# Kernel optimization log

Hardware: AMD Instinct MI355X
Metric: run time of the kernel (lower is better)

## Reference

```python
import jax, jax.numpy as jnp
import numpy as np

B, T, L = 64, 60, 49
EMBED, HID, VOCAB = 768, 768, 10000


def setup_inputs() -> dict:
    key = jax.random.key(0)
    ks = jax.random.split(key, 17)
    def n(k, shape, s=1.0):
        return jax.random.normal(k, shape, dtype=jnp.float32) * s
    W = 0.02  # param init scale
    return {
        "x": n(ks[0], (B, T, 2 * EMBED)),
        "hiddens": n(ks[1], (B, T, HID)),
        "cells": n(ks[2], (B, T, HID)),
        "G": n(ks[3], (B, L, HID)),
        "H": n(ks[4], (B, L, HID)),
        # Sentinel params (bias=False)
        "W_sx": n(ks[5], (HID, 2 * EMBED), W),
        "W_sh": n(ks[6], (HID, HID), W),
        # SwitchableAttention params
        "W_ax": n(ks[7], (HID, 2 * EMBED), W),
        "W_ah": n(ks[8], (HID, HID), W),
        "W_ag": n(ks[9], (HID, HID), W),
        "w_switch": n(ks[10], (1, HID), W),
        # Atten (adaptive attention) params, bias=False
        "Wv": n(ks[11], (L, HID), W),
        "Wg": n(ks[12], (L, HID), W),
        "Ws": n(ks[13], (L, HID), W),
        "wh": n(ks[14], (1, L), W),
        # output MLP
        "W_mlp": n(ks[15], (VOCAB, HID), W),
        "b_mlp": jnp.zeros((VOCAB,), dtype=jnp.float32),
    }


def reference(x, hiddens, cells, G, H, W_sx, W_sh, W_ax, W_ah, W_ag,
              w_switch, Wv, Wg, Ws, wh, W_mlp, b_mlp):
    # Dropout layers are treated as identity (eval mode).
    b, t, _ = x.shape
    # h_{t-1}: zero initial hidden prepended, last step dropped
    h0 = jnp.zeros((b, 1, HID), dtype=hiddens.dtype)
    hiddens_t_1 = jnp.concatenate([h0, hiddens[:, :-1, :]], axis=1)

    # Sentinel gate: sigmoid(Wx x + Wh h_{t-1}) * tanh(c_t)
    gate = jax.nn.sigmoid(jnp.einsum('bte,he->bth', x, W_sx)
                          + jnp.einsum('btk,hk->bth', hiddens_t_1, W_sh))
    s_t = gate * jnp.tanh(cells)  # [B,T,HID]

    # SwitchableAttention: gate between visual H and guidance G per region,
    # conditioned on pooled word context x.
    q = jnp.einsum('bte,he->bth', x, W_ax).mean(axis=1)  # [B,HID]
    sH = jnp.einsum('blh,oh->blo', jnp.tanh(jnp.einsum('blh,kh->blk', H, W_ah) + q[:, None, :]), w_switch)  # [B,L,1]
    sG = jnp.einsum('blh,oh->blo', jnp.tanh(jnp.einsum('blh,kh->blk', G, W_ag) + q[:, None, :]), w_switch)  # [B,L,1]
    switch_weights = jax.nn.softmax(jnp.concatenate([sH, sG], axis=-1), axis=-1)  # [B,L,2]
    V = switch_weights[..., 0:1] * H + switch_weights[..., 1:2] * G  # [B,L,HID]

    # Adaptive attention (Atten): spatial attention + visual sentinel
    pv = jnp.einsum('blh,kh->blk', V, Wv)        # [B,L,49]
    pg = jnp.einsum('bth,kh->btk', hiddens, Wg)  # [B,T,49]
    z_t = jnp.einsum('btlk,ok->btlo', jnp.tanh(pv[:, None, :, :] + pg[:, :, None, :]), wh)[..., 0]  # [B,T,L]
    alpha = jax.nn.softmax(z_t, axis=-1)  # [B,T,L]
    z_s = jnp.einsum('btk,ok->bto', jnp.tanh(jnp.einsum('bth,kh->btk', s_t, Ws) + pg), wh)  # [B,T,1]
    alpha_hat = jax.nn.softmax(jnp.concatenate([z_t, z_s], axis=-1), axis=-1)  # [B,T,L+1]
    beta = alpha_hat[..., -1:]  # [B,T,1]
    c_t = jnp.einsum('btl,blh->bth', alpha, V)
    c_hat = beta * s_t + (1.0 - beta) * c_t

    scores = jnp.einsum('bth,vh->btv', c_hat + hiddens, W_mlp) + b_mlp  # [B,T,VOCAB]
    return scores, alpha, beta, switch_weights
```

## Files before the change

### kernel.cpp

```cpp
#include <hip/hip_runtime.h>

#define BB 64
#define TT 60
#define LL 49
#define HID 768
#define E2 1536
#define K2 2304
#define VOC 10000
#define BT (BB*TT)
#define BL (BB*LL)
#define NPAD_MLP 10240
#define NPAD_S 128

typedef __bf16 bf16x8 __attribute__((ext_vector_type(8)));
typedef float f32x4 __attribute__((ext_vector_type(4)));

__device__ __forceinline__ unsigned short f2bf(float f) {
  union { float f; unsigned int u; } v; v.f = f;
  unsigned int u = v.u;
  return (unsigned short)((u + 0x7fffu + ((u >> 16) & 1u)) >> 16);
}
__device__ __forceinline__ float bf2f(unsigned short h) {
  union { unsigned int u; float f; } v; v.u = ((unsigned int)h) << 16;
  return v.f;
}
__device__ __forceinline__ float fast_tanh(float x) {
  float e = __expf(2.f * x);
  return 1.f - 2.f / (e + 1.f);
}
__device__ __forceinline__ float fast_sigmoid(float x) {
  return 1.f / (1.f + __expf(-x));
}

#define NSEG 14
#define CHUNK4 2048
struct SegT {
  const float* src;
  unsigned short* dst;
  int n4, rl4, dstride4, dcol4, nrows, mode, blk0;
};
struct SegTable { SegT s[NSEG]; };

__global__ __launch_bounds__(256) void k_convall(SegTable tab) {
  int b = blockIdx.x;
  int si = 0;
#pragma unroll
  for (int i = 1; i < NSEG; ++i) si += (b >= tab.s[i].blk0);
  SegT sg = tab.s[si];
  int lb = b - sg.blk0;
  int end = (lb + 1) * CHUNK4; end = end < sg.n4 ? end : sg.n4;
  for (int i = lb * CHUNK4 + threadIdx.x; i < end; i += 256) {
    int row = i / sg.rl4, c = i - row * sg.rl4;
    ushort4 o; o.x = o.y = o.z = o.w = 0;
    if (sg.mode == 0) {
      float4 v = ((const float4*)sg.src)[i];
      o.x = f2bf(v.x); o.y = f2bf(v.y); o.z = f2bf(v.z); o.w = f2bf(v.w);
    } else if (sg.mode == 1) {
      if (row < sg.nrows) {
        float4 v = ((const float4*)sg.src)[i];
        o.x = f2bf(v.x); o.y = f2bf(v.y); o.z = f2bf(v.z); o.w = f2bf(v.w);
      }
    } else {
      if (row % TT != 0) {
        float4 v = ((const float4*)sg.src)[i - sg.rl4];
        o.x = f2bf(v.x); o.y = f2bf(v.y); o.z = f2bf(v.z); o.w = f2bf(v.w);
      }
    }
    ((ushort4*)sg.dst)[(size_t)row * sg.dstride4 + sg.dcol4 + c] = o;
  }
}

__global__ __launch_bounds__(256) void k_xmean(const float* __restrict__ x,
                                               unsigned short* __restrict__ xm) {
  int b = blockIdx.x / 6;
  int c = (blockIdx.x % 6) * 256 + threadIdx.x;
  float s = 0.f;
  for (int t = 0; t < TT; ++t) s += x[((size_t)b * TT + t) * E2 + c];
  xm[(size_t)b * E2 + c] = f2bf(s * (1.f / 60.f));
}

struct SSeg {
  const unsigned short* A; const unsigned short* B;
  float* C; const float* bias; const float* aux; unsigned short* outbf;
  int M, Nout, K, nMblk, blk0, emode;
};
#define NSSEG 4
struct SSegTable { SSeg s[NSSEG]; };

__global__ __launch_bounds__(256) void gemm_bt64_seg(SSegTable tab)
{
  __shared__ __attribute__((aligned(16))) unsigned short As[128*32];
  __shared__ __attribute__((aligned(16))) unsigned short Bs[64*32];
  const int tid  = threadIdx.x;
  const int lane = tid & 63;
  const int wave = tid >> 6;

  const int nwg = gridDim.x;
  const int id  = blockIdx.x;
  const int q = nwg >> 3, r = nwg & 7;
  const int xcd = id & 7, lo = id >> 3;
  const int wgid = (xcd < r ? xcd * (q + 1) : r * (q + 1) + (xcd - r) * q) + lo;

  int si = 0;
#pragma unroll
  for (int i = 1; i < NSSEG; ++i) si += (wgid >= tab.s[i].blk0);
  const SSeg sg = tab.s[si];
  const int lwg = wgid - sg.blk0;
  const int mb = lwg % sg.nMblk;
  const int nb = lwg / sg.nMblk;
  const int M = sg.M, Nout = sg.Nout, K = sg.K;
  const unsigned short* __restrict__ A  = sg.A;
  const unsigned short* __restrict__ Bw = sg.B;
  const int m0 = mb * 128;
  const int n0 = nb * 64;
  const int wm = (wave & 1) * 64;
  const int wn = (wave >> 1) * 32;

  f32x4 acc[4][2];
#pragma unroll
  for (int i = 0; i < 4; ++i)
#pragma unroll
    for (int j = 0; j < 2; ++j) acc[i][j] = f32x4{0.f, 0.f, 0.f, 0.f};

  const int lrow = lane & 15;
  const int kb   = (lane >> 4) * 8;

  for (int k0 = 0; k0 < K; k0 += 32) {
    __syncthreads();
#pragma unroll
    for (int p = 0; p < 2; ++p) {
      int slot = p * 256 + wave * 64 + lane;
      int row = slot >> 2, c8 = slot & 3;
      int ar = m0 + row; ar = ar < M ? ar : (M - 1);
      const unsigned short* asrc = A + (size_t)ar * K + k0 + c8 * 8;
      __builtin_amdgcn_global_load_lds(
          (const __attribute__((address_space(1))) void*)asrc,
          (__attribute__((address_space(3))) void*)&As[slot * 8],
          16, 0, 0);
    }
    {
      int slot = wave * 64 + lane;
      int row = slot >> 2, c8 = slot & 3;
      const unsigned short* bsrc = Bw + (size_t)(n0 + row) * K + k0 + c8 * 8;
      __builtin_amdgcn_global_load_lds(
          (const __attribute__((address_space(1))) void*)bsrc,
          (__attribute__((address_space(3))) void*)&Bs[slot * 8],
          16, 0, 0);
    }
    __syncthreads();

    bf16x8 av[4], bv[2];
#pragma unroll
    for (int i = 0; i < 4; ++i)
      av[i] = *(const bf16x8*)&As[(wm + i * 16 + lrow) * 32 + kb];
#pragma unroll
    for (int j = 0; j < 2; ++j)
      bv[j] = *(const bf16x8*)&Bs[(wn + j * 16 + lrow) * 32 + kb];
#pragma unroll
    for (int i = 0; i < 4; ++i)
#pragma unroll
      for (int j = 0; j < 2; ++j)
        acc[i][j] = __builtin_amdgcn_mfma_f32_16x16x32_bf16(av[i], bv[j], acc[i][j], 0, 0, 0);
  }

  const int cr = (lane >> 4) * 4;
  const int cc = lane & 15;
  if (sg.emode == 0) {
    float* __restrict__ C = sg.C;
    const float* __restrict__ bias = sg.bias;
#pragma unroll
    for (int i = 0; i < 4; ++i) {
      int row0 = m0 + wm + i * 16 + cr;
#pragma unroll
      for (int j = 0; j < 2; ++j) {
        int col = n0 + wn + j * 16 + cc;
        if (col < Nout) {
          float badd = bias ? bias[col] : 0.f;
#pragma unroll
          for (int r2 = 0; r2 < 4; ++r2) {
            int row = row0 + r2;
            if (row < M) C[(size_t)row * Nout + col] = acc[i][j][r2] + badd;
          }
        }
      }
    }
  } else if (sg.emode == 1) {
    const float* __restrict__ cells = sg.aux;
    unsigned short* __restrict__ ob = sg.outbf;
#pragma unroll
    for (int i = 0; i < 4; ++i) {
      int row0 = m0 + wm + i * 16 + cr;
#pragma unroll
      for (int j = 0; j < 2; ++j) {
        int col = n0 + wn + j * 16 + cc;
        if (col < Nout) {
#pragma unroll
          for (int r2 = 0; r2 < 4; ++r2) {
            int row = row0 + r2;
            if (row < M) {
              float cv = cells[(size_t)row * Nout + col];
              ob[(size_t)row * Nout + col] = f2bf(fast_sigmoid(acc[i][j][r2]) * fast_tanh(cv));
            }
          }
        }
      }
    }
  } else {
    unsigned short* __restrict__ ob = sg.outbf;
#pragma unroll
    for (int i = 0; i < 4; ++i) {
      int row0 = m0 + wm + i * 16 + cr;
#pragma unroll
      for (int j = 0; j < 2; ++j) {
        int col = n0 + wn + j * 16 + cc;
        if (col < Nout) {
#pragma unroll
          for (int r2 = 0; r2 < 4; ++r2) {
            int row = row0 + r2;
            if (row < M) ob[(size_t)row * Nout + col] = f2bf(acc[i][j][r2]);
          }
        }
      }
    }
  }
}

#define VM6() asm volatile("s_waitcnt vmcnt(6)" ::: "memory")
#define VM0() asm volatile("s_waitcnt vmcnt(0)" ::: "memory")
#define BARR() do { asm volatile("" ::: "memory"); __builtin_amdgcn_s_barrier(); \
                    asm volatile("" ::: "memory"); } while (0)

#define SC_STAGE(bufi, kt) do {                                                 \
  int k0_ = (kt) * 32;                                                          \
  _Pragma("unroll")                                                             \
  for (int l_ = 0; l_ < 2; ++l_) {                                              \
    int rr_ = l_ * 64 + wave * 16 + (lane >> 2);                                \
    int ss_ = (lane & 3) ^ ((rr_ >> 1) & 3);                                    \
    const unsigned short* src_ = Ap + (size_t)(m0 + rr_) * K + k0_ + ss_ * 8;   \
    char* dst_ = smem + (bufi) * 24576 + l_ * 4096 + wave * 1024;               \
    __builtin_amdgcn_global_load_lds(                                           \
        (const __attribute__((address_space(1))) void*)src_,                    \
        (__attribute__((address_space(3))) void*)dst_, 16, 0, 0);               \
  }                                                                             \
  _Pragma("unroll")                                                             \
  for (int l_ = 0; l_ < 4; ++l_) {                                              \
    int rr_ = l_ * 64 + wave * 16 + (lane >> 2);                                \
    int ss_ = (lane & 3) ^ ((rr_ >> 1) & 3);                                    \
    const unsigned short* src_ = Bw + (size_t)(n0 + rr_) * K + k0_ + ss_ * 8;   \
    char* dst_ = smem + (bufi) * 24576 + 8192 + l_ * 4096 + wave * 1024;        \
    __builtin_amdgcn_global_load_lds(                                           \
        (const __attribute__((address_space(1))) void*)src_,                    \
        (__attribute__((address_space(3))) void*)dst_, 16, 0, 0);               \
  }                                                                             \
} while (0)

#define SC_LDA(bufi, row) (*(const bf16x8*)(smem + (bufi) * 24576 + (row) * 64 + ((cg ^ (((row) >> 1) & 3)) * 16)))
#define SC_LDB(bufi, row) (*(const bf16x8*)(smem + (bufi) * 24576 + 8192 + (row) * 64 + ((cg ^ (((row) >> 1) & 3)) * 16)))

#define SC_TILE(bufi, STAGE_STMT, VM_STMT) do {                                 \
  STAGE_STMT;                                                                   \
  bf16x8 afr0 = SC_LDA(bufi, wm + lrow);                                        \
  bf16x8 afr1 = SC_LDA(bufi, wm + 16 + lrow);                                   \
  bf16x8 afr2 = SC_LDA(bufi, wm + 32 + lrow);                                   \
  bf16x8 afr3 = SC_LDA(bufi, wm + 48 + lrow);                                   \
  __builtin_amdgcn_s_setprio(1);                                                \
  _Pragma("unroll")                                                             \
  for (int j_ = 0; j_ < 8; ++j_) {                                              \
    bf16x8 b_ = SC_LDB(bufi, wn + j_ * 16 + lrow);                              \
    acc[0][j_] = __builtin_amdgcn_mfma_f32_16x16x32_bf16(afr0, b_, acc[0][j_], 0, 0, 0); \
    acc[1][j_] = __builtin_amdgcn_mfma_f32_16x16x32_bf16(afr1, b_, acc[1][j_], 0, 0, 0); \
    acc[2][j_] = __builtin_amdgcn_mfma_f32_16x16x32_bf16(afr2, b_, acc[2][j_], 0, 0, 0); \
    acc[3][j_] = __builtin_amdgcn_mfma_f32_16x16x32_bf16(afr3, b_, acc[3][j_], 0, 0, 0); \
  }                                                                             \
  __builtin_amdgcn_s_setprio(0);                                                \
  VM_STMT;                                                                      \
  BARR();                                                                       \
} while (0)

__global__ __launch_bounds__(256, 2) void gemm_sc2(
    const unsigned short* __restrict__ Ap,
    const unsigned short* __restrict__ Bw,
    float* __restrict__ C,
    const float* __restrict__ bias,
    int M, int Nout, int K, int nMblk)
{
  extern __shared__ char smem[];
  const int tid  = threadIdx.x;
  const int lane = tid & 63;
  const int wave = tid >> 6;
  const int lrow = lane & 15;
  const int cg   = lane >> 4;

  const int nwg = gridDim.x;
  const int id  = blockIdx.x;
  const int q = nwg >> 3, r = nwg & 7;
  const int xcd = id & 7, lo = id >> 3;
  const int wgid = (xcd < r ? xcd * (q + 1) : r * (q + 1) + (xcd - r) * q) + lo;
  const int mb = wgid % nMblk;
  const int nb = wgid / nMblk;

  const int m0 = mb * 128;
  const int n0 = nb * 256;
  const int wm = (wave >> 1) * 64;
  const int wn = (wave & 1) * 128;

  f32x4 acc[4][8];
#pragma unroll
  for (int i = 0; i < 4; ++i)
#pragma unroll
    for (int j = 0; j < 8; ++j) acc[i][j] = f32x4{0.f, 0.f, 0.f, 0.f};

  const int NT = K >> 5;

  SC_STAGE(0, 0);
  SC_STAGE(1, 1);
  VM6();
  BARR();

  int b = 0;
  for (int kt = 0; kt < NT - 2; ++kt) {
    int b2 = b + 2; if (b2 >= 3) b2 -= 3;
    SC_TILE(b, SC_STAGE(b2, kt + 2), VM6(););
    ++b; if (b == 3) b = 0;
  }
  SC_TILE(b, ;, VM0(););
  ++b; if (b == 3) b = 0;
  SC_TILE(b, ;, ;);

#pragma unroll
  for (int i = 0; i < 4; ++i) {
    int row0 = m0 + wm + i * 16 + (lane >> 4) * 4;
#pragma unroll
    for (int j = 0; j < 8; ++j) {
      int col = n0 + wn + j * 16 + (lane & 15);
      if (col < Nout) {
        float badd = bias ? bias[col] : 0.f;
#pragma unroll
        for (int r2 = 0; r2 < 4; ++r2)
          C[(size_t)(row0 + r2) * Nout + col] = acc[i][j][r2] + badd;
      }
    }
  }
}

__global__ __launch_bounds__(256) void k_switch(
    const unsigned short* __restrict__ AH, const unsigned short* __restrict__ AG,
    const float* __restrict__ q, const float* __restrict__ wsw,
    const float* __restrict__ H, const float* __restrict__ G,
    unsigned short* __restrict__ Vbf, float* __restrict__ sw_out)
{
  int bl = blockIdx.x;
  int b = bl / LL;
  int tid = threadIdx.x;
  float aH = 0.f, aG = 0.f;
  for (int h = tid; h < HID; h += 256) {
    float qv = q[b * HID + h], w = wsw[h];
    aH += fast_tanh(bf2f(AH[(size_t)bl * HID + h]) + qv) * w;
    aG += fast_tanh(bf2f(AG[(size_t)bl * HID + h]) + qv) * w;
  }
#pragma unroll
  for (int off = 32; off > 0; off >>= 1) {
    aH += __shfl_down(aH, off);
    aG += __shfl_down(aG, off);
  }
  __shared__ float redH[4], redG[4];
  int lane = tid & 63, wave = tid >> 6;
  if (lane == 0) { redH[wave] = aH; redG[wave] = aG; }
  __syncthreads();
  float sH = redH[0] + redH[1] + redH[2] + redH[3];
  float sG = redG[0] + redG[1] + redG[2] + redG[3];
  float m = fmaxf(sH, sG);
  float e0 = __expf(sH - m), e1 = __expf(sG - m);
  float inv = 1.f / (e0 + e1);
  float sw0 = e0 * inv, sw1 = e1 * inv;
  if (tid == 0) { sw_out[bl * 2] = sw0; sw_out[bl * 2 + 1] = sw1; }
  for (int h = tid; h < HID; h += 256) {
    float v = sw0 * H[(size_t)bl * HID + h] + sw1 * G[(size_t)bl * HID + h];
    Vbf[(size_t)bl * HID + h] = f2bf(v);
  }
}

__global__ __launch_bounds__(256) void k_attn(
    const float* __restrict__ PV, const float* __restrict__ PG,
    const float* __restrict__ SS, const float* __restrict__ wh,
    const unsigned short* __restrict__ stbf, const unsigned short* __restrict__ Vbf,
    const float* __restrict__ hiddens,
    float* __restrict__ alpha_out, float* __restrict__ beta_out,
    unsigned short* __restrict__ chh)
{
  const int TG = 4;
  int b  = blockIdx.x / (TT / TG);
  int t0 = (blockIdx.x % (TT / TG)) * TG;
  int tid = threadIdx.x;
  __shared__ float pg_s[TG][LL], wh_s[LL], zz[TG][LL + 1], alpha_s[TG][LL], beta_sh[TG];

  if (tid < LL) wh_s[tid] = wh[tid];
  if (tid < TG * LL) {
    int tt = tid / LL, k = tid - tt * LL;
    pg_s[tt][k] = PG[(size_t)(b * TT + t0 + tt) * 64 + k];
  }
  __syncthreads();

  if (tid < TG * (LL + 1)) {
    int tt = tid / (LL + 1), l = tid - tt * (LL + 1);
    const float* src = (l < LL) ? &PV[((size_t)b * LL + l) * 64]
                                : &SS[(size_t)(b * TT + t0 + tt) * 64];
    float acc = 0.f;
    for (int k = 0; k < LL; ++k) acc += fast_tanh(src[k] + pg_s[tt][k]) * wh_s[k];
    zz[tt][l] = acc;
  }
  __syncthreads();

  if (tid < TG) {
    int tt = tid, bt = b * TT + t0 + tt;
    float mx = -1e30f;
    for (int l = 0; l < LL; ++l) mx = fmaxf(mx, zz[tt][l]);
    float sum = 0.f;
    for (int l = 0; l < LL; ++l) { float e = __expf(zz[tt][l] - mx); alpha_s[tt][l] = e; sum += e; }
    float inv = 1.f / sum;
    for (int l = 0; l < LL; ++l) {
      alpha_s[tt][l] *= inv;
      alpha_out[(size_t)bt * LL + l] = alpha_s[tt][l];
    }
    float mx2 = fmaxf(mx, zz[tt][LL]);
    float s2 = 0.f;
    for (int l = 0; l <= LL; ++l) s2 += __expf(zz[tt][l] - mx2);
    float bet = __expf(zz[tt][LL] - mx2) / s2;
    beta_sh[tt] = bet;
    beta_out[bt] = bet;
  }
  __syncthreads();

  for (int h = tid; h < HID; h += 256) {
    float ct[TG] = {0.f, 0.f, 0.f, 0.f};
    for (int l = 0; l < LL; ++l) {
      float v = bf2f(Vbf[((size_t)b * LL + l) * HID + h]);
#pragma unroll
      for (int tt = 0; tt < TG; ++tt) ct[tt] += alpha_s[tt][l] * v;
    }
#pragma unroll
    for (int tt = 0; tt < TG; ++tt) {
      int bt = b * TT + t0 + tt;
      float bet = beta_sh[tt];
      float s = bf2f(stbf[(size_t)bt * HID + h]);
      float chat = bet * s + (1.f - bet) * ct[tt];
      chh[(size_t)bt * HID + h] = f2bf(chat + hiddens[(size_t)bt * HID + h]);
    }
  }
}

extern "C" void kernel_launch(void* const* d_in, const int* in_sizes, int n_in,
                              void* d_out, int out_size, void* d_ws, size_t ws_size,
                              hipStream_t stream)
{
  const float* x       = (const float*)d_in[0];
  const float* hiddens = (const float*)d_in[1];
  const float* cells   = (const float*)d_in[2];
  const float* G       = (const float*)d_in[3];
  const float* H       = (const float*)d_in[4];
  const float* W_sx    = (const float*)d_in[5];
  const float* W_sh    = (const float*)d_in[6];
  const float* W_ax    = (const float*)d_in[7];
  const float* W_ah    = (const float*)d_in[8];
  const float* W_ag    = (const float*)d_in[9];
  const float* w_sw    = (const float*)d_in[10];
  const float* Wv      = (const float*)d_in[11];
  const float* Wg      = (const float*)d_in[12];
  const float* Ws      = (const float*)d_in[13];
  const float* wh      = (const float*)d_in[14];
  const float* W_mlp   = (const float*)d_in[15];
  const float* b_mlp   = (const float*)d_in[16];

  float* scores = (float*)d_out;
  float* alpha  = scores + (size_t)BT * VOC;
  float* beta   = alpha + (size_t)BT * LL;
  float* swout  = beta + BT;

  char* wsp = (char*)d_ws;
  size_t off = 0;
  auto alloc = [&](size_t bytes) -> char* {
    char* p = wsp + off;
    off += (bytes + 255) & ~(size_t)255;
    return p;
  };

  unsigned short* xh     = (unsigned short*)alloc((size_t)BT * K2 * 2);
  unsigned short* wsxh   = (unsigned short*)alloc((size_t)HID * K2 * 2);
  unsigned short* waxb   = (unsigned short*)alloc((size_t)HID * E2 * 2);
  unsigned short* wahb   = (unsigned short*)alloc((size_t)HID * HID * 2);
  unsigned short* wagb   = (unsigned short*)alloc((size_t)HID * HID * 2);
  unsigned short* Hbf    = (unsigned short*)alloc((size_t)BL * HID * 2);
  unsigned short* Gbf    = (unsigned short*)alloc((size_t)BL * HID * 2);
  unsigned short* hidbf  = (unsigned short*)alloc((size_t)BT * HID * 2);
  unsigned short* wvb    = (unsigned short*)alloc((size_t)NPAD_S * HID * 2);
  unsigned short* wgb    = (unsigned short*)alloc((size_t)NPAD_S * HID * 2);
  unsigned short* wsb    = (unsigned short*)alloc((size_t)NPAD_S * HID * 2);
  unsigned short* wmlpb  = (unsigned short*)alloc((size_t)NPAD_MLP * HID * 2);
  unsigned short* Vbf    = (unsigned short*)alloc((size_t)BL * HID * 2);
  unsigned short* stbf   = (unsigned short*)alloc((size_t)BT * HID * 2);
  unsigned short* chh    = (unsigned short*)alloc((size_t)BT * HID * 2);
  unsigned short* xmbf   = (unsigned short*)alloc((size_t)BB * E2 * 2);
  unsigned short* AH     = (unsigned short*)alloc((size_t)BL * HID * 2);
  unsigned short* AG     = (unsigned short*)alloc((size_t)BL * HID * 2);
  float* qb = (float*)alloc((size_t)BB * HID * 4);
  float* PV = (float*)alloc((size_t)BL * 64 * 4);
  float* PG = (float*)alloc((size_t)BT * 64 * 4);
  float* SS = (float*)alloc((size_t)BT * 64 * 4);
  (void)ws_size; (void)in_sizes; (void)n_in; (void)out_size;

  SegTable tab;
  int blk = 0, si = 0;
  auto seg = [&](const float* s, unsigned short* d, int n4, int rl4, int dstride4,
                 int dcol4, int nrows, int mode) {
    tab.s[si].src = s; tab.s[si].dst = d; tab.s[si].n4 = n4; tab.s[si].rl4 = rl4;
    tab.s[si].dstride4 = dstride4; tab.s[si].dcol4 = dcol4;
    tab.s[si].nrows = nrows; tab.s[si].mode = mode; tab.s[si].blk0 = blk;
    blk += (n4 + CHUNK4 - 1) / CHUNK4; ++si;
  };
  seg(W_sx,    wsxh,  HID * 384, 384, 576, 0,   0, 0);
  seg(W_sh,    wsxh,  HID * 192, 192, 576, 384, 0, 0);
  seg(x,       xh,    BT * 384,  384, 576, 0,   0, 0);
  seg(hiddens, xh,    BT * 192,  192, 576, 384, 0, 2);
  seg(W_ax,    waxb,  HID * 384, 384, 384, 0,   0, 0);
  seg(W_ah,    wahb,  HID * 192, 192, 192, 0,   0, 0);
  seg(W_ag,    wagb,  HID * 192, 192, 192, 0,   0, 0);
  seg(H,       Hbf,   BL * 192,  192, 192, 0,   0, 0);
  seg(G,       Gbf,   BL * 192,  192, 192, 0,   0, 0);
  seg(hiddens, hidbf, BT * 192,  192, 192, 0,   0, 0);
  seg(Wv,      wvb,   NPAD_S * 192, 192, 192, 0, LL, 1);
  seg(Wg,      wgb,   NPAD_S * 192, 192, 192, 0, LL, 1);
  seg(Ws,      wsb,   NPAD_S * 192, 192, 192, 0, LL, 1);
  seg(W_mlp,   wmlpb, NPAD_MLP * 192, 192, 192, 0, VOC, 1);
  k_convall<<<blk, 256, 0, stream>>>(tab);

  k_xmean<<<BB * 6, 256, 0, stream>>>(x, xmbf);

  SSegTable mt;
  mt.s[0] = SSeg{xh,   wsxh, nullptr, nullptr, cells, stbf, BT, HID, K2,  30, 0,   1};
  mt.s[1] = SSeg{Hbf,  wahb, nullptr, nullptr, nullptr, AH, BL, HID, HID, 25, 360, 2};
  mt.s[2] = SSeg{Gbf,  wagb, nullptr, nullptr, nullptr, AG, BL, HID, HID, 25, 660, 2};
  mt.s[3] = SSeg{xmbf, waxb, qb,      nullptr, nullptr, nullptr, BB, HID, E2,  1,  960, 0};
  gemm_bt64_seg<<<972, 256, 0, stream>>>(mt);

  k_switch<<<BL, 256, 0, stream>>>(AH, AG, qb, w_sw, H, G, Vbf, swout);

  SSegTable st;
  st.s[0] = SSeg{Vbf,   wvb, PV, nullptr, nullptr, nullptr, BL, 64, HID, 25, 0,  0};
  st.s[1] = SSeg{hidbf, wgb, PG, nullptr, nullptr, nullptr, BT, 64, HID, 30, 25, 0};
  st.s[2] = SSeg{stbf,  wsb, SS, nullptr, nullptr, nullptr, BT, 64, HID, 30, 55, 0};
  st.s[3] = st.s[2]; st.s[3].blk0 = 0x7fffffff;
  gemm_bt64_seg<<<85, 256, 0, stream>>>(st);

  k_attn<<<BB * (TT / 4), 256, 0, stream>>>(PV, PG, SS, wh, stbf, Vbf, hiddens,
                                            alpha, beta, chh);

  gemm_sc2<<<30 * 40, 256, 73728, stream>>>(chh, wmlpb, scores, b_mlp, BT, VOC, HID, 30);
}
```

Measured before the change: 300.8 us.

## Replace 128x64 segmented GEMM with double-buffered 128x128 tile kernel

Adds a new segmented GEMM kernel, gemm_p128, that computes 128x128 output tiles. It stages A and B into swizzled LDS through a two-buffer global_load_lds pipeline and splits each k-step into two MFMA phases, raising wave priority during the MFMAs. It replaces the earlier 972-block launch for the sentinel, switch-attention and query GEMMs, halving the block count and doubling output reuse per tile. In exchange each thread holds more accumulator registers, there are fewer blocks for load balance, and A rows past M are clamped.

```diff
diff --git a/kernel.cpp b/kernel.cpp
--- a/kernel.cpp
+++ b/kernel.cpp
@@ -165,6 +165,154 @@
 
   const int cr = (lane >> 4) * 4;
   const int cc = lane & 15;
+  float* __restrict__ C = sg.C;
+#pragma unroll
+  for (int i = 0; i < 4; ++i) {
+    int row0 = m0 + wm + i * 16 + cr;
+#pragma unroll
+    for (int j = 0; j < 2; ++j) {
+      int col = n0 + wn + j * 16 + cc;
+      if (col < Nout) {
+#pragma unroll
+        for (int r2 = 0; r2 < 4; ++r2) {
+          int row = row0 + r2;
+          if (row < M) C[(size_t)row * Nout + col] = acc[i][j][r2];
+        }
+      }
+    }
+  }
+}
+
+#define BARR() do { asm volatile("" ::: "memory"); __builtin_amdgcn_s_barrier(); \
+                    asm volatile("" ::: "memory"); } while (0)
+#define VM2() asm volatile("s_waitcnt vmcnt(2)" ::: "memory")
+#define VM0() asm volatile("s_waitcnt vmcnt(0)" ::: "memory")
+#define VM6() asm volatile("s_waitcnt vmcnt(6)" ::: "memory")
+
+struct GSeg {
+  const unsigned short* A; const unsigned short* B;
+  float* C; const float* bias; const float* aux; unsigned short* outbf;
+  int M, Nout, K, nMblk, blk0, emode;
+};
+#define NGSEG 5
+struct GSegTable { GSeg s[NGSEG]; };
+
+#define P128_ST(bufi, op, kt) do {                                              \
+  int k0_ = (kt) * 32;                                                          \
+  _Pragma("unroll")                                                             \
+  for (int l_ = 0; l_ < 2; ++l_) {                                              \
+    int slot_ = l_ * 256 + tid;                                                 \
+    int row_ = slot_ >> 2;                                                      \
+    int ss_ = (slot_ & 3) ^ ((row_ >> 1) & 3);                                  \
+    int gr_;                                                                    \
+    if (op) gr_ = n0 + row_;                                                    \
+    else { gr_ = m0 + row_; gr_ = gr_ < M ? gr_ : (M - 1); }                    \
+    const unsigned short* src_ = ((op) ? Bw : Ap) + (size_t)gr_ * K + k0_ + ss_ * 8; \
+    char* dst_ = smem + (bufi) * 16384 + (op) * 8192 + slot_ * 16;              \
+    __builtin_amdgcn_global_load_lds(                                           \
+        (const __attribute__((address_space(1))) void*)src_,                    \
+        (__attribute__((address_space(3))) void*)dst_, 16, 0, 0);               \
+  }                                                                             \
+} while (0)
+
+#define P128_LDA(bufi, row) (*(const bf16x8*)(smem + (bufi) * 16384 + (row) * 64 + ((cg ^ (((row) >> 1) & 3)) * 16)))
+#define P128_LDB(bufi, row) (*(const bf16x8*)(smem + (bufi) * 16384 + 8192 + (row) * 64 + ((cg ^ (((row) >> 1) & 3)) * 16)))
+
+#define P128_PH0(bufi, STAGE_STMT) do {                                         \
+  STAGE_STMT;                                                                   \
+  bf16x8 bfr0 = P128_LDB(bufi, wn + lrow);                                      \
+  bf16x8 bfr1 = P128_LDB(bufi, wn + 16 + lrow);                                 \
+  _Pragma("unroll")                                                             \
+  for (int i_ = 0; i_ < 4; ++i_) afr[i_] = P128_LDA(bufi, wm + i_ * 16 + lrow); \
+  __builtin_amdgcn_s_setprio(1);                                                \
+  _Pragma("unroll")                                                             \
+  for (int i_ = 0; i_ < 4; ++i_) {                                              \
+    acc[i_][0] = __builtin_amdgcn_mfma_f32_16x16x32_bf16(afr[i_], bfr0, acc[i_][0], 0, 0, 0); \
+    acc[i_][1] = __builtin_amdgcn_mfma_f32_16x16x32_bf16(afr[i_], bfr1, acc[i_][1], 0, 0, 0); \
+  }                                                                             \
+  __builtin_amdgcn_s_setprio(0);                                                \
+  BARR();                                                                       \
+} while (0)
+
+#define P128_PH1(bufi, STAGE_STMT, VM_STMT) do {                                \
+  STAGE_STMT;                                                                   \
+  bf16x8 bfr0 = P128_LDB(bufi, wn + 32 + lrow);                                 \
+  bf16x8 bfr1 = P128_LDB(bufi, wn + 48 + lrow);                                 \
+  __builtin_amdgcn_s_setprio(1);                                                \
+  _Pragma("unroll")                                                             \
+  for (int i_ = 0; i_ < 4; ++i_) {                                              \
+    acc[i_][2] = __builtin_amdgcn_mfma_f32_16x16x32_bf16(afr[i_], bfr0, acc[i_][2], 0, 0, 0); \
+    acc[i_][3] = __builtin_amdgcn_mfma_f32_16x16x32_bf16(afr[i_], bfr1, acc[i_][3], 0, 0, 0); \
+  }                                                                             \
+  __builtin_amdgcn_s_setprio(0);                                                \
+  VM_STMT;                                                                      \
+  BARR();                                                                       \
+} while (0)
+
+__global__ __launch_bounds__(256, 3) void gemm_p128(GSegTable tab)
+{
+  extern __shared__ char smem[];
+  const int tid  = threadIdx.x;
+  const int lane = tid & 63;
+  const int wave = tid >> 6;
+  const int lrow = lane & 15;
+  const int cg   = lane >> 4;
+
+  const int nwg = gridDim.x;
+  const int id  = blockIdx.x;
+  const int q = nwg >> 3, r = nwg & 7;
+  const int xcd = id & 7, lo = id >> 3;
+  const int wgid = (xcd < r ? xcd * (q + 1) : r * (q + 1) + (xcd - r) * q) + lo;
+
+  int si = 0;
+#pragma unroll
+  for (int i = 1; i < NGSEG; ++i) si += (wgid >= tab.s[i].blk0);
+  const GSeg sg = tab.s[si];
+  const int lwg = wgid - sg.blk0;
+  const int mb = lwg % sg.nMblk;
+  const int nb = lwg / sg.nMblk;
+  const int M = sg.M, Nout = sg.Nout, K = sg.K;
+  const unsigned short* __restrict__ Ap = sg.A;
+  const unsigned short* __restrict__ Bw = sg.B;
+
+  const int m0 = mb * 128;
+  const int n0 = nb * 128;
+  const int wm = (wave >> 1) * 64;
+  const int wn = (wave & 1) * 64;
+
+  f32x4 acc[4][4];
+#pragma unroll
+  for (int i = 0; i < 4; ++i)
+#pragma unroll
+    for (int j = 0; j < 4; ++j) acc[i][j] = f32x4{0.f, 0.f, 0.f, 0.f};
+  bf16x8 afr[4];
+
+  const int NT = K >> 5;
+
+  P128_ST(0, 0, 0);
+  P128_ST(0, 1, 0);
+  P128_ST(1, 0, 1);
+  VM2();
+  BARR();
+
+  for (int kt = 0; kt < NT - 2; ++kt) {
+    const int c = kt & 1;
+    P128_PH0(c, P128_ST(c ^ 1, 1, kt + 1));
+    P128_PH1(c, P128_ST(c, 0, kt + 2), VM2(););
+  }
+  {
+    const int c = (NT - 2) & 1;
+    P128_PH0(c, P128_ST(c ^ 1, 1, NT - 1));
+    P128_PH1(c, ;, VM0(););
+  }
+  {
+    const int c = (NT - 1) & 1;
+    P128_PH0(c, ;);
+    P128_PH1(c, ;, ;);
+  }
+
+  const int cr = (lane >> 4) * 4;
+  const int cc = lane & 15;
   if (sg.emode == 0) {
     float* __restrict__ C = sg.C;
     const float* __restrict__ bias = sg.bias;
@@ -172,7 +320,7 @@
     for (int i = 0; i < 4; ++i) {
       int row0 = m0 + wm + i * 16 + cr;
 #pragma unroll
-      for (int j = 0; j < 2; ++j) {
+      for (int j = 0; j < 4; ++j) {
         int col = n0 + wn + j * 16 + cc;
         if (col < Nout) {
           float badd = bias ? bias[col] : 0.f;
@@ -191,7 +339,7 @@
     for (int i = 0; i < 4; ++i) {
       int row0 = m0 + wm + i * 16 + cr;
 #pragma unroll
-      for (int j = 0; j < 2; ++j) {
+      for (int j = 0; j < 4; ++j) {
         int col = n0 + wn + j * 16 + cc;
         if (col < Nout) {
 #pragma unroll
@@ -211,7 +359,7 @@
     for (int i = 0; i < 4; ++i) {
       int row0 = m0 + wm + i * 16 + cr;
 #pragma unroll
-      for (int j = 0; j < 2; ++j) {
+      for (int j = 0; j < 4; ++j) {
         int col = n0 + wn + j * 16 + cc;
         if (col < Nout) {
 #pragma unroll
@@ -224,11 +372,6 @@
     }
   }
 }
-
-#define VM6() asm volatile("s_waitcnt vmcnt(6)" ::: "memory")
-#define VM0() asm volatile("s_waitcnt vmcnt(0)" ::: "memory")
-#define BARR() do { asm volatile("" ::: "memory"); __builtin_amdgcn_s_barrier(); \
-                    asm volatile("" ::: "memory"); } while (0)
 
 #define SC_STAGE(bufi, kt) do {                                                 \
   int k0_ = (kt) * 32;                                                          \
@@ -535,12 +678,13 @@
 
   k_xmean<<<BB * 6, 256, 0, stream>>>(x, xmbf);
 
-  SSegTable mt;
-  mt.s[0] = SSeg{xh,   wsxh, nullptr, nullptr, cells, stbf, BT, HID, K2,  30, 0,   1};
-  mt.s[1] = SSeg{Hbf,  wahb, nullptr, nullptr, nullptr, AH, BL, HID, HID, 25, 360, 2};
-  mt.s[2] = SSeg{Gbf,  wagb, nullptr, nullptr, nullptr, AG, BL, HID, HID, 25, 660, 2};
-  mt.s[3] = SSeg{xmbf, waxb, qb,      nullptr, nullptr, nullptr, BB, HID, E2,  1,  960, 0};
-  gemm_bt64_seg<<<972, 256, 0, stream>>>(mt);
+  GSegTable mt;
+  mt.s[0] = GSeg{xh,   wsxh, nullptr, nullptr, cells,   stbf,    BT, HID, K2,  30, 0,   1};
+  mt.s[1] = GSeg{Hbf,  wahb, nullptr, nullptr, nullptr, AH,      BL, HID, HID, 25, 180, 2};
+  mt.s[2] = GSeg{Gbf,  wagb, nullptr, nullptr, nullptr, AG,      BL, HID, HID, 25, 330, 2};
+  mt.s[3] = GSeg{xmbf, waxb, qb,      nullptr, nullptr, nullptr, BB, HID, E2,  1,  480, 0};
+  mt.s[4] = mt.s[3]; mt.s[4].blk0 = 0x7fffffff;
+  gemm_p128<<<486, 256, 32768, stream>>>(mt);
 
   k_switch<<<BL, 256, 0, stream>>>(AH, AG, qb, w_sw, H, G, Vbf, swout);
 
```

Result: faster. 293.6 us (-2.4%).
